# Performance work log

Measured on AMD Instinct MI355X. Metric: run time of the kernel, lower is better.

## Reference

```python
import jax, jax.numpy as jnp
import numpy as np

B, T, C = 4, 2048, 1024
H, HS = 16, 64  # num_heads, head_size; H*HS == C

def setup_inputs() -> dict:
    key = jax.random.key(0)
    ks = jax.random.split(key, 6)
    s = 0.02
    x = jax.random.normal(ks[0], (B, T, C), dtype=jnp.float32)
    Wq = jax.random.normal(ks[1], (H, C, HS), dtype=jnp.float32) * s
    Wk = jax.random.normal(ks[2], (H, C, HS), dtype=jnp.float32) * s
    Wv = jax.random.normal(ks[3], (H, C, HS), dtype=jnp.float32) * s
    Wproj = jax.random.normal(ks[4], (C, C), dtype=jnp.float32) * s  # applied as out @ Wproj
    bproj = jax.random.normal(ks[5], (C,), dtype=jnp.float32) * s
    return {"x": x, "Wq": Wq, "Wk": Wk, "Wv": Wv, "Wproj": Wproj, "bproj": bproj}

def reference(x, Wq, Wk, Wv, Wproj, bproj):
    Bx, Tx, Cx = x.shape
    scale = Cx ** (-0.5)  # NOTE: original scales by n_embd, not head_size
    q = jnp.einsum('btc,hcd->bhtd', x, Wq)
    k = jnp.einsum('btc,hcd->bhtd', x, Wk)
    v = jnp.einsum('btc,hcd->bhtd', x, Wv)
    wei = jnp.einsum('bhtd,bhsd->bhts', q, k) * scale  # [B,H,T,T]
    causal = jnp.tril(jnp.ones((Tx, Tx), dtype=bool))
    wei = jnp.where(causal, wei, -jnp.inf)
    wei = jax.nn.softmax(wei, axis=-1)
    out = jnp.einsum('bhts,bhsd->bhtd', wei, v)
    out = out.transpose(0, 2, 1, 3).reshape(Bx, Tx, Cx)  # concat heads
    return out @ Wproj + bproj
```

## Files before the change

kernel.cpp:

```cpp
#include <hip/hip_runtime.h>


using u16    = unsigned short;
using bf16x8 = __attribute__((ext_vector_type(8))) short;
using bf16x4 = __attribute__((ext_vector_type(4))) short;
using f32x4  = __attribute__((ext_vector_type(4))) float;

#define MFMA_BF16(a, b, c) __builtin_amdgcn_mfma_f32_16x16x32_bf16((a), (b), (c), 0, 0, 0)

__device__ __forceinline__ f32x4 mfma16(bf16x4 a, bf16x4 b, f32x4 c) {
#if __has_builtin(__builtin_amdgcn_mfma_f32_16x16x16bf16_1k)
    return __builtin_amdgcn_mfma_f32_16x16x16bf16_1k(a, b, c, 0, 0, 0);
#elif __has_builtin(__builtin_amdgcn_mfma_f32_16x16x16_bf16)
    return __builtin_amdgcn_mfma_f32_16x16x16_bf16(a, b, c, 0, 0, 0);
#else
    asm("v_mfma_f32_16x16x16_bf16 %0, %1, %2, %0" : "+v"(c) : "v"(a), "v"(b));
    return c;
#endif
}

__device__ __forceinline__ u16 f2bf(float f) {
    union { float f; unsigned u; } v; v.f = f;
    unsigned u = v.u;
    u += 0x7FFFu + ((u >> 16) & 1u);
    return (u16)(u >> 16);
}
__device__ __forceinline__ short tbf(float f) {
    union { float f; unsigned u; } v; v.f = f;
    return (short)(v.u >> 16);
}

__device__ __forceinline__ void gl_lds16(const void* g, void* s) {
    __builtin_amdgcn_global_load_lds(
        (__attribute__((address_space(1))) void*)g,
        (__attribute__((address_space(3))) void*)s,
        16, 0, 0);
}

__global__ void cvt_x(const float* __restrict__ x, u16* __restrict__ xb, int n4) {
    int i = blockIdx.x * blockDim.x + threadIdx.x;
    if (i < n4) {
        float4 v = ((const float4*)x)[i];
        ushort4 o;
        o.x = f2bf(v.x); o.y = f2bf(v.y); o.z = f2bf(v.z); o.w = f2bf(v.w);
        ((ushort4*)xb)[i] = o;
    }
}

__global__ void transpose_w(const float* __restrict__ Wq, const float* __restrict__ Wk,
                            const float* __restrict__ Wv, u16* __restrict__ WT) {
    __shared__ float tile[64][65];
    const int tid = threadIdx.x;
    const int c0  = blockIdx.x * 64;
    const int h   = blockIdx.y;
    const int z   = blockIdx.z;
    const float* W = (z == 0 ? Wq : (z == 1 ? Wk : Wv)) + (size_t)h * 1024 * 64;
    u16* out = WT + (size_t)z * 1024 * 1024 + (size_t)h * 64 * 1024;
    #pragma unroll
    for (int i = 0; i < 16; ++i) {
        int idx = i * 256 + tid;
        int r = idx >> 6, d = idx & 63;
        tile[d][r] = W[(size_t)(c0 + r) * 64 + d];
    }
    __syncthreads();
    #pragma unroll
    for (int i = 0; i < 16; ++i) {
        int idx = i * 256 + tid;
        int d = idx >> 6, j = idx & 63;
        out[(size_t)d * 1024 + c0 + j] = f2bf(tile[d][j]);
    }
}

__global__ void transpose_p(const float* __restrict__ Wp, u16* __restrict__ WpT) {
    __shared__ float tile[64][65];
    const int tid = threadIdx.x;
    const int c0  = blockIdx.x * 64;
    const int n0  = blockIdx.y * 64;
    #pragma unroll
    for (int i = 0; i < 16; ++i) {
        int idx = i * 256 + tid;
        int r = idx >> 6, j = idx & 63;
        tile[j][r] = Wp[(size_t)(c0 + r) * 1024 + n0 + j];
    }
    __syncthreads();
    #pragma unroll
    for (int i = 0; i < 16; ++i) {
        int idx = i * 256 + tid;
        int r = idx >> 6, j = idx & 63;
        WpT[(size_t)(n0 + r) * 1024 + c0 + j] = f2bf(tile[r][j]);
    }
}

template <int MODE>
__global__ __launch_bounds__(256, 2)
void gemm_bt(const u16* __restrict__ A, const u16* __restrict__ Bt,
             u16* __restrict__ Oq, u16* __restrict__ Ok, u16* __restrict__ Ov,
             float* __restrict__ Op, const float* __restrict__ bias) {
    constexpr int K = 1024;
    __shared__ u16 As[128 * 32];
    __shared__ u16 Bs[128 * 32];
    const int tid  = threadIdx.x;
    const int w    = tid >> 6;
    const int lane = tid & 63;
    const int quad = lane >> 4;
    const int l16  = lane & 15;
    const int m0   = blockIdx.x * 128;
    const int n0   = blockIdx.y * 128;
    const u16* Bp  = (MODE == 0) ? (Bt + (size_t)blockIdx.z * 1024 * 1024) : Bt;

    const f32x4 zero = {0.f, 0.f, 0.f, 0.f};
    f32x4 acc[4][4];
    #pragma unroll
    for (int i = 0; i < 4; ++i)
        #pragma unroll
        for (int j = 0; j < 4; ++j) acc[i][j] = zero;

    const int wr = (w >> 1) * 64;
    const int wc = (w & 1) * 64;

    for (int k0 = 0; k0 < K; k0 += 32) {
        __syncthreads();
        #pragma unroll
        for (int i = 0; i < 2; ++i) {
            int c = i * 256 + tid;
            int row = c >> 2, ko = (c & 3) * 8;
            gl_lds16(A + (size_t)(m0 + row) * K + (k0 + ko), &As[(i * 256 + w * 64) * 8]);
        }
        #pragma unroll
        for (int i = 0; i < 2; ++i) {
            int c = i * 256 + tid;
            int row = c >> 2, ko = (c & 3) * 8;
            gl_lds16(Bp + (size_t)(n0 + row) * K + (k0 + ko), &Bs[(i * 256 + w * 64) * 8]);
        }
        __syncthreads();
        bf16x8 af[4], bfr[4];
        #pragma unroll
        for (int i = 0; i < 4; ++i)
            af[i] = *(const bf16x8*)&As[(wr + i * 16 + l16) * 32 + quad * 8];
        #pragma unroll
        for (int j = 0; j < 4; ++j)
            bfr[j] = *(const bf16x8*)&Bs[(wc + j * 16 + l16) * 32 + quad * 8];
        #pragma unroll
        for (int i = 0; i < 4; ++i)
            #pragma unroll
            for (int j = 0; j < 4; ++j)
                acc[i][j] = MFMA_BF16(af[i], bfr[j], acc[i][j]);
    }

    #pragma unroll
    for (int i = 0; i < 4; ++i) {
        #pragma unroll
        for (int j = 0; j < 4; ++j) {
            #pragma unroll
            for (int r = 0; r < 4; ++r) {
                const int m = m0 + wr + i * 16 + quad * 4 + r;
                const int n = n0 + wc + j * 16 + l16;
                const float v = acc[i][j][r];
                if (MODE == 0) {
                    const int b = m >> 11, t = m & 2047;
                    const int h = n >> 6, d = n & 63;
                    const int bh = b * 16 + h;
                    if (blockIdx.z == 0)
                        Oq[((size_t)bh * 2048 + t) * 64 + d] = f2bf(v * 0.03125f);
                    else if (blockIdx.z == 1)
                        Ok[((size_t)bh * 2048 + t) * 64 + d] = f2bf(v);
                    else
                        Ov[((size_t)bh * 64 + d) * 2048 + t] = f2bf(v);
                } else {
                    Op[(size_t)m * 1024 + n] = v + bias[n];
                }
            }
        }
    }
}

__global__ __launch_bounds__(256, 2)
void attn7(const u16* __restrict__ Q, const u16* __restrict__ Kg,
           const u16* __restrict__ Vt, u16* __restrict__ O) {
    __shared__ __align__(16) u16 Ks[2][2 * 128 * 32];
    __shared__ __align__(16) u16 VF[16 * 128 * 4];
    const int tid  = threadIdx.x;
    const int w    = tid >> 6;
    const int lane = tid & 63;
    const int quad = lane >> 4;
    const int l16  = lane & 15;
    const int bh   = blockIdx.y;
    const u16* Qp = Q  + (size_t)bh * 2048 * 64;
    const u16* Kp = Kg + (size_t)bh * 2048 * 64;
    const u16* Vp = Vt + (size_t)bh * 64 * 2048;
    const int b = bh >> 4, h = bh & 15;
    const float NEG_INF = -__builtin_inff();
    const f32x4 zero = {0.f, 0.f, 0.f, 0.f};
    const int vd = w * 16 + l16;

    #pragma unroll
    for (int ph = 0; ph < 2; ++ph) {
        const int tt = ph ? (int)blockIdx.x : 15 - (int)blockIdx.x;
        const int t0 = tt * 128;
        const int ns = tt + 1;

        bf16x8 bq[2][2];
        #pragma unroll
        for (int tf = 0; tf < 2; ++tf)
            #pragma unroll
            for (int kk = 0; kk < 2; ++kk)
                bq[tf][kk] = *(const bf16x8*)(Qp + (size_t)(t0 + w * 32 + tf * 16 + l16) * 64
                                              + kk * 32 + quad * 8);

        f32x4 oacc[4][2];
        float lsum[2] = {0.f, 0.f};
        #pragma unroll
        for (int df = 0; df < 4; ++df)
            #pragma unroll
            for (int tf = 0; tf < 2; ++tf) oacc[df][tf] = zero;

        __syncthreads();
        uint4 vr[4];
        #pragma unroll
        for (int i = 0; i < 4; ++i) {
            int c = i * 256 + tid;
            int kk = c >> 9, row = (c >> 2) & 127, q4 = c & 3;
            gl_lds16(Kp + (size_t)row * 64 + kk * 32 + q4 * 8,
                     &Ks[0][(size_t)(i * 256 + w * 64) * 8]);
        }
        #pragma unroll
        for (int r = 0; r < 4; ++r)
            vr[r] = *(const uint4*)(Vp + (size_t)vd * 2048 + (r * 4 + quad) * 8);

        for (int it = 0; it < ns; ++it) {
            const int s0 = it * 128;
            const u16* Kc = Ks[it & 1];
            __syncthreads();
            #pragma unroll
            for (int r = 0; r < 4; ++r) {
                const int uA = ((w * 4 + r) * 128) + (quad & 1) * 64 + l16 * 2
                               + ((quad >> 1) & 1);
                *(uint2*)&VF[(size_t)uA * 4]        = make_uint2(vr[r].x, vr[r].y);
                *(uint2*)&VF[(size_t)(uA + 32) * 4] = make_uint2(vr[r].z, vr[r].w);
            }
            __syncthreads();

            if (it + 1 < ns) {
                const int sn = s0 + 128;
                u16* Kn = Ks[(it + 1) & 1];
                #pragma unroll
                for (int i = 0; i < 4; ++i) {
                    int c = i * 256 + tid;
                    int kk = c >> 9, row = (c >> 2) & 127, q4 = c & 3;
                    gl_lds16(Kp + (size_t)(sn + row) * 64 + kk * 32 + q4 * 8,
                             &Kn[(size_t)(i * 256 + w * 64) * 8]);
                }
                #pragma unroll
                for (int r = 0; r < 4; ++r)
                    vr[r] = *(const uint4*)(Vp + (size_t)vd * 2048 + sn + (r * 4 + quad) * 8);
            }

            const bool diag = (it == ns - 1);
            bf16x4 bp[8][2];
            #pragma unroll
            for (int st = 0; st < 8; ++st) {
                bf16x8 ak0 = *(const bf16x8*)&Kc[(st * 16 + l16) * 32 + quad * 8];
                bf16x8 ak1 = *(const bf16x8*)&Kc[(128 * 32) + (st * 16 + l16) * 32 + quad * 8];
                #pragma unroll
                for (int tf = 0; tf < 2; ++tf) {
                    f32x4 s = MFMA_BF16(ak0, bq[tf][0], zero);
                    s = MFMA_BF16(ak1, bq[tf][1], s);
                    if (diag) {
                        #pragma unroll
                        for (int r = 0; r < 4; ++r) {
                            int ss = s0 + st * 16 + quad * 4 + r;
                            int t  = t0 + w * 32 + tf * 16 + l16;
                            if (ss > t) s[r] = NEG_INF;
                        }
                    }
                    float p0 = __expf(s[0]), p1 = __expf(s[1]);
                    float p2 = __expf(s[2]), p3 = __expf(s[3]);
                    lsum[tf] += (p0 + p1) + (p2 + p3);
                    bf16x4 bb; bb[0] = tbf(p0); bb[1] = tbf(p1);
                    bb[2] = tbf(p2); bb[3] = tbf(p3);
                    bp[st][tf] = bb;
                }
            }
            #pragma unroll
            for (int kcp = 0; kcp < 4; ++kcp)
                #pragma unroll
                for (int df = 0; df < 4; ++df) {
                    bf16x8 av = *(const bf16x8*)&VF[(size_t)(((df * 4 + kcp) * 128)
                                                    + quad * 32 + l16 * 2) * 4];
                    bf16x4 alo = __builtin_shufflevector(av, av, 0, 1, 2, 3);
                    bf16x4 ahi = __builtin_shufflevector(av, av, 4, 5, 6, 7);
                    #pragma unroll
                    for (int tf = 0; tf < 2; ++tf) {
                        oacc[df][tf] = mfma16(alo, bp[2 * kcp][tf], oacc[df][tf]);
                        oacc[df][tf] = mfma16(ahi, bp[2 * kcp + 1][tf], oacc[df][tf]);
                    }
                }
        }

        #pragma unroll
        for (int tf = 0; tf < 2; ++tf) {
            float s = lsum[tf];
            s += __shfl_xor(s, 16, 64);
            s += __shfl_xor(s, 32, 64);
            lsum[tf] = 1.0f / s;
        }
        #pragma unroll
        for (int df = 0; df < 4; ++df)
            #pragma unroll
            for (int tf = 0; tf < 2; ++tf)
                #pragma unroll
                for (int r = 0; r < 4; ++r) {
                    int t = t0 + w * 32 + tf * 16 + l16;
                    int d = df * 16 + quad * 4 + r;
                    O[((size_t)(b * 2048 + t)) * 1024 + h * 64 + d]
                        = f2bf(oacc[df][tf][r] * lsum[tf]);
                }
    }
}

extern "C" void kernel_launch(void* const* d_in, const int* in_sizes, int n_in,
                              void* d_out, int out_size, void* d_ws, size_t ws_size,
                              hipStream_t stream) {
    const float* x  = (const float*)d_in[0];
    const float* Wq = (const float*)d_in[1];
    const float* Wk = (const float*)d_in[2];
    const float* Wv = (const float*)d_in[3];
    const float* Wp = (const float*)d_in[4];
    const float* bp = (const float*)d_in[5];
    float* out = (float*)d_out;

    char* ws = (char*)d_ws;
    u16* Xb  = (u16*)(ws);
    u16* Xo  = (u16*)(ws);
    u16* WT  = (u16*)(ws + (16ull << 20));
    u16* WpT = (u16*)(ws + (22ull << 20));
    u16* Qw  = (u16*)(ws + (24ull << 20));
    u16* Kw  = (u16*)(ws + (40ull << 20));
    u16* Vw  = (u16*)(ws + (56ull << 20));

    cvt_x<<<8192, 256, 0, stream>>>(x, Xb, 8192 * 1024 / 4);
    transpose_w<<<dim3(16, 16, 3), 256, 0, stream>>>(Wq, Wk, Wv, WT);
    transpose_p<<<dim3(16, 16), 256, 0, stream>>>(Wp, WpT);
    gemm_bt<0><<<dim3(64, 8, 3), 256, 0, stream>>>(Xb, WT, Qw, Kw, Vw, nullptr, nullptr);
    attn7<<<dim3(8, 64), 256, 0, stream>>>(Qw, Kw, Vw, Xo);
    gemm_bt<1><<<dim3(64, 8, 1), 256, 0, stream>>>(Xo, WpT, nullptr, nullptr, nullptr, out, bp);
}
```

Baseline: 265.6 us.

## Stage V and attention outputs through LDS, swizzle K, use exp2 and MFMA row sums

The V projection epilogue now transposes its tile through swizzled shared memory so the transposed output is written as 16-byte vectors instead of scattered 2-byte stores. The attention output does the same through the VF buffer. The K tile in LDS gets an XOR swizzle to reduce bank conflicts on the fragment loads. Softmax switches from exp to exp2, with log2(e) folded into the Q scale, and the row sums are computed by an MFMA against a ones vector instead of scalar adds and shuffles. These changes add extra barriers and shared-memory round trips, and the row sum is now taken from bf16-rounded probabilities.

```diff
diff --git a/kernel.cpp b/kernel.cpp
--- a/kernel.cpp
+++ b/kernel.cpp
@@ -2,6 +2,7 @@
 
 
 using u16    = unsigned short;
+using u32    = unsigned int;
 using bf16x8 = __attribute__((ext_vector_type(8))) short;
 using bf16x4 = __attribute__((ext_vector_type(4))) short;
 using f32x4  = __attribute__((ext_vector_type(4))) float;
@@ -29,6 +30,13 @@
     union { float f; unsigned u; } v; v.f = f;
     return (short)(v.u >> 16);
 }
+__device__ __forceinline__ float fexp2(float x) {
+#if __has_builtin(__builtin_amdgcn_exp2f)
+    return __builtin_amdgcn_exp2f(x);
+#else
+    return exp2f(x);
+#endif
+}
 
 __device__ __forceinline__ void gl_lds16(const void* g, void* s) {
     __builtin_amdgcn_global_load_lds(
@@ -97,8 +105,9 @@
              u16* __restrict__ Oq, u16* __restrict__ Ok, u16* __restrict__ Ov,
              float* __restrict__ Op, const float* __restrict__ bias) {
     constexpr int K = 1024;
-    __shared__ u16 As[128 * 32];
-    __shared__ u16 Bs[128 * 32];
+    __shared__ u16 SH[2][128 * 32];
+    u16* As = SH[0];
+    u16* Bs = SH[1];
     const int tid  = threadIdx.x;
     const int w    = tid >> 6;
     const int lane = tid & 63;
@@ -147,27 +156,58 @@
                 acc[i][j] = MFMA_BF16(af[i], bfr[j], acc[i][j]);
     }
 
-    #pragma unroll
-    for (int i = 0; i < 4; ++i) {
-        #pragma unroll
-        for (int j = 0; j < 4; ++j) {
-            #pragma unroll
-            for (int r = 0; r < 4; ++r) {
-                const int m = m0 + wr + i * 16 + quad * 4 + r;
-                const int n = n0 + wc + j * 16 + l16;
-                const float v = acc[i][j][r];
-                if (MODE == 0) {
-                    const int b = m >> 11, t = m & 2047;
-                    const int h = n >> 6, d = n & 63;
-                    const int bh = b * 16 + h;
-                    if (blockIdx.z == 0)
-                        Oq[((size_t)bh * 2048 + t) * 64 + d] = f2bf(v * 0.03125f);
-                    else if (blockIdx.z == 1)
-                        Ok[((size_t)bh * 2048 + t) * 64 + d] = f2bf(v);
-                    else
-                        Ov[((size_t)bh * 64 + d) * 2048 + t] = f2bf(v);
-                } else {
-                    Op[(size_t)m * 1024 + n] = v + bias[n];
+    if (MODE == 0 && blockIdx.z == 2) {
+        u32* buf = (u32*)SH;
+        const int bh0 = (m0 >> 11) * 16;
+        #pragma unroll
+        for (int mh = 0; mh < 2; ++mh) {
+            __syncthreads();
+            if ((w >> 1) == mh) {
+                #pragma unroll
+                for (int i = 0; i < 4; ++i)
+                    #pragma unroll
+                    for (int j = 0; j < 4; ++j)
+                        #pragma unroll
+                        for (int rp = 0; rp < 2; ++rp) {
+                            const int nl = wc + j * 16 + l16;
+                            const int t2 = i * 8 + quad * 2 + rp;
+                            const u32 lo = f2bf(acc[i][j][2 * rp]);
+                            const u32 hi = f2bf(acc[i][j][2 * rp + 1]);
+                            buf[nl * 32 + (t2 ^ ((nl & 7) << 2))] = lo | (hi << 16);
+                        }
+            }
+            __syncthreads();
+            const int nl = tid >> 1, half = tid & 1;
+            const int h = (n0 + nl) >> 6, d = (n0 + nl) & 63;
+            u16* orow = Ov + ((size_t)(bh0 + h) * 64 + d) * 2048 + (m0 & 2047) + mh * 64;
+            #pragma unroll
+            for (int c = 0; c < 4; ++c) {
+                const int d2b = half * 16 + c * 4;
+                uint4 vv = *(const uint4*)&buf[nl * 32 + (d2b ^ ((nl & 7) << 2))];
+                *(uint4*)(orow + d2b * 2) = vv;
+            }
+        }
+    } else {
+        #pragma unroll
+        for (int i = 0; i < 4; ++i) {
+            #pragma unroll
+            for (int j = 0; j < 4; ++j) {
+                #pragma unroll
+                for (int r = 0; r < 4; ++r) {
+                    const int m = m0 + wr + i * 16 + quad * 4 + r;
+                    const int n = n0 + wc + j * 16 + l16;
+                    const float v = acc[i][j][r];
+                    if (MODE == 0) {
+                        const int b = m >> 11, t = m & 2047;
+                        const int h = n >> 6, d = n & 63;
+                        const int bh = b * 16 + h;
+                        if (blockIdx.z == 0)
+                            Oq[((size_t)bh * 2048 + t) * 64 + d] = f2bf(v * 0.0450842203f);
+                        else
+                            Ok[((size_t)bh * 2048 + t) * 64 + d] = f2bf(v);
+                    } else {
+                        Op[(size_t)m * 1024 + n] = v + bias[n];
+                    }
                 }
             }
         }
@@ -175,7 +215,7 @@
 }
 
 __global__ __launch_bounds__(256, 2)
-void attn7(const u16* __restrict__ Q, const u16* __restrict__ Kg,
+void attn8(const u16* __restrict__ Q, const u16* __restrict__ Kg,
            const u16* __restrict__ Vt, u16* __restrict__ O) {
     __shared__ __align__(16) u16 Ks[2][2 * 128 * 32];
     __shared__ __align__(16) u16 VF[16 * 128 * 4];
@@ -191,7 +231,10 @@
     const int b = bh >> 4, h = bh & 15;
     const float NEG_INF = -__builtin_inff();
     const f32x4 zero = {0.f, 0.f, 0.f, 0.f};
+    const short ONE = (short)0x3F80;
+    const bf16x4 vones = {ONE, ONE, ONE, ONE};
     const int vd = w * 16 + l16;
+    const int ksw = ((l16 >> 3) & 1) << 4;
 
     #pragma unroll
     for (int ph = 0; ph < 2; ++ph) {
@@ -208,7 +251,7 @@
                                               + kk * 32 + quad * 8);
 
         f32x4 oacc[4][2];
-        float lsum[2] = {0.f, 0.f};
+        f32x4 lacc[2] = {zero, zero};
         #pragma unroll
         for (int df = 0; df < 4; ++df)
             #pragma unroll
@@ -219,8 +262,9 @@
         #pragma unroll
         for (int i = 0; i < 4; ++i) {
             int c = i * 256 + tid;
-            int kk = c >> 9, row = (c >> 2) & 127, q4 = c & 3;
-            gl_lds16(Kp + (size_t)row * 64 + kk * 32 + q4 * 8,
+            int kk = c >> 9, row = (c >> 2) & 127;
+            int q4s = (c & 3) ^ (((row >> 3) & 1) << 1);
+            gl_lds16(Kp + (size_t)row * 64 + kk * 32 + q4s * 8,
                      &Ks[0][(size_t)(i * 256 + w * 64) * 8]);
         }
         #pragma unroll
@@ -246,8 +290,9 @@
                 #pragma unroll
                 for (int i = 0; i < 4; ++i) {
                     int c = i * 256 + tid;
-                    int kk = c >> 9, row = (c >> 2) & 127, q4 = c & 3;
-                    gl_lds16(Kp + (size_t)(sn + row) * 64 + kk * 32 + q4 * 8,
+                    int kk = c >> 9, row = (c >> 2) & 127;
+                    int q4s = (c & 3) ^ (((row >> 3) & 1) << 1);
+                    gl_lds16(Kp + (size_t)(sn + row) * 64 + kk * 32 + q4s * 8,
                              &Kn[(size_t)(i * 256 + w * 64) * 8]);
                 }
                 #pragma unroll
@@ -259,8 +304,9 @@
             bf16x4 bp[8][2];
             #pragma unroll
             for (int st = 0; st < 8; ++st) {
-                bf16x8 ak0 = *(const bf16x8*)&Kc[(st * 16 + l16) * 32 + quad * 8];
-                bf16x8 ak1 = *(const bf16x8*)&Kc[(128 * 32) + (st * 16 + l16) * 32 + quad * 8];
+                const int kbase = (st * 16 + l16) * 32 + quad * 8;
+                bf16x8 ak0 = *(const bf16x8*)&Kc[kbase ^ ksw];
+                bf16x8 ak1 = *(const bf16x8*)&Kc[(128 * 32) + (kbase ^ ksw)];
                 #pragma unroll
                 for (int tf = 0; tf < 2; ++tf) {
                     f32x4 s = MFMA_BF16(ak0, bq[tf][0], zero);
@@ -273,14 +319,18 @@
                             if (ss > t) s[r] = NEG_INF;
                         }
                     }
-                    float p0 = __expf(s[0]), p1 = __expf(s[1]);
-                    float p2 = __expf(s[2]), p3 = __expf(s[3]);
-                    lsum[tf] += (p0 + p1) + (p2 + p3);
+                    float p0 = fexp2(s[0]), p1 = fexp2(s[1]);
+                    float p2 = fexp2(s[2]), p3 = fexp2(s[3]);
                     bf16x4 bb; bb[0] = tbf(p0); bb[1] = tbf(p1);
                     bb[2] = tbf(p2); bb[3] = tbf(p3);
                     bp[st][tf] = bb;
                 }
             }
+            #pragma unroll
+            for (int st = 0; st < 8; ++st)
+                #pragma unroll
+                for (int tf = 0; tf < 2; ++tf)
+                    lacc[tf] = mfma16(vones, bp[st][tf], lacc[tf]);
             #pragma unroll
             for (int kcp = 0; kcp < 4; ++kcp)
                 #pragma unroll
@@ -297,24 +347,33 @@
                 }
         }
 
-        #pragma unroll
-        for (int tf = 0; tf < 2; ++tf) {
-            float s = lsum[tf];
-            s += __shfl_xor(s, 16, 64);
-            s += __shfl_xor(s, 32, 64);
-            lsum[tf] = 1.0f / s;
-        }
-        #pragma unroll
-        for (int df = 0; df < 4; ++df)
-            #pragma unroll
-            for (int tf = 0; tf < 2; ++tf)
-                #pragma unroll
-                for (int r = 0; r < 4; ++r) {
-                    int t = t0 + w * 32 + tf * 16 + l16;
-                    int d = df * 16 + quad * 4 + r;
-                    O[((size_t)(b * 2048 + t)) * 1024 + h * 64 + d]
-                        = f2bf(oacc[df][tf][r] * lsum[tf]);
+        __syncthreads();
+        {
+            u32* ob = (u32*)VF;
+            const float inv[2] = {1.0f / lacc[0][0], 1.0f / lacc[1][0]};
+            #pragma unroll
+            for (int df = 0; df < 4; ++df)
+                #pragma unroll
+                for (int tf = 0; tf < 2; ++tf) {
+                    const int tl = w * 32 + tf * 16 + l16;
+                    #pragma unroll
+                    for (int rp = 0; rp < 2; ++rp) {
+                        const u32 lo = f2bf(oacc[df][tf][2 * rp]     * inv[tf]);
+                        const u32 hi = f2bf(oacc[df][tf][2 * rp + 1] * inv[tf]);
+                        const int d2 = df * 8 + quad * 2 + rp;
+                        ob[tl * 32 + (d2 ^ ((tl & 7) << 2))] = lo | (hi << 16);
+                    }
                 }
+            __syncthreads();
+            const int tl = tid >> 1, half = tid & 1;
+            u16* orow = O + ((size_t)(b * 2048 + t0 + tl)) * 1024 + h * 64;
+            #pragma unroll
+            for (int c = 0; c < 4; ++c) {
+                const int d2b = half * 16 + c * 4;
+                uint4 vv = *(const uint4*)&ob[tl * 32 + (d2b ^ ((tl & 7) << 2))];
+                *(uint4*)(orow + d2b * 2) = vv;
+            }
+        }
     }
 }
 
@@ -342,6 +401,6 @@
     transpose_w<<<dim3(16, 16, 3), 256, 0, stream>>>(Wq, Wk, Wv, WT);
     transpose_p<<<dim3(16, 16), 256, 0, stream>>>(Wp, WpT);
     gemm_bt<0><<<dim3(64, 8, 3), 256, 0, stream>>>(Xb, WT, Qw, Kw, Vw, nullptr, nullptr);
-    attn7<<<dim3(8, 64), 256, 0, stream>>>(Qw, Kw, Vw, Xo);
+    attn8<<<dim3(8, 64), 256, 0, stream>>>(Qw, Kw, Vw, Xo);
     gemm_bt<1><<<dim3(64, 8, 1), 256, 0, stream>>>(Xo, WpT, nullptr, nullptr, nullptr, out, bp);
 }
```

After: 254.6 us. -4.1%, faster.
